# Optimization experiments

Hardware: AMD Instinct MI355X
Metric: run time of the kernel (lower is better)

The kernel has to match this reference:

```python
import jax, jax.numpy as jnp
import numpy as np

CH = 64          # channels
OC = 64          # out_channels
B, H, W = 8, 128, 128
NCA_C = CH + OC  # 128, NCA state channels
K = 3            # kernel_size
DILS = (1, 2, 4, 8)
HID = 64         # NCA update hidden
EPS = 1e-5


def setup_inputs() -> dict:
    key = jax.random.key(0)
    ks = jax.random.split(key, 16)
    def n(k, shape, s=0.02):
        return jax.random.normal(k, shape, jnp.float32) * s
    return {
        "x": jax.random.normal(ks[0], (B, H, W, CH), jnp.float32),
        "c": jax.random.normal(ks[1], (B, OC), jnp.float32),
        # Attention params
        "Wq": n(ks[2], (CH, OC)), "bq": jnp.zeros((OC,), jnp.float32),
        "Wk": n(ks[3], (OC, OC)), "bk": jnp.zeros((OC,), jnp.float32),
        "Wv": n(ks[4], (OC, OC)), "bv": jnp.zeros((OC,), jnp.float32),
        "Wo": n(ks[5], (OC, OC)), "bo": jnp.zeros((OC,), jnp.float32),
        "ln_g": jnp.ones((OC,), jnp.float32), "ln_b": jnp.zeros((OC,), jnp.float32),
        # NCA depthwise perception kernels, one per dilation: [4, NCA_C, 1, K, K]
        "pk": n(ks[6], (len(DILS), NCA_C, 1, K, K), 0.1),
        # NCA update MLP
        "W1": n(ks[7], ((1 + len(DILS)) * NCA_C, HID)), "b1": jnp.zeros((HID,), jnp.float32),
        "W2": n(ks[8], (HID, CH)), "b2": jnp.zeros((CH,), jnp.float32),
    }


def _layernorm(z, g, b):
    m = jnp.mean(z, axis=-1, keepdims=True)
    v = jnp.var(z, axis=-1, keepdims=True)
    return (z - m) / jnp.sqrt(v + EPS) * g + b


def _forward(x, c, Wq, bq, Wk, bk, Wv, bv, Wo, bo, ln_g, ln_b, pk, W1, b1, W2, b2):
    b_, h_, w_, _ = x.shape
    # ---- Attention(x, c): single-key softmax pooling over H*W ----
    q = x.reshape(b_, h_ * w_, CH) @ Wq + bq              # [B, HW, OC]
    k = c @ Wk + bk                                        # [B, OC]
    v = c @ Wv + bv                                        # [B, OC]
    scores = jnp.einsum('bno,bo->bn', q, k) * (OC ** -0.5)  # [B, HW]
    attn = jax.nn.softmax(scores, axis=1)                  # softmax over spatial dim
    attended = jnp.einsum('bn,bo->bo', attn, v)            # weighted pool (weights sum to 1)
    a = _layernorm(attended @ Wo + bo + c, ln_g, ln_b)     # out_proj + residual + LN
    c2 = c + a                                             # outer residual in NCAAttention

    # ---- concat broadcast context -> NCA state [B,H,W,NCA_C] ----
    c_exp = jnp.broadcast_to(c2[:, None, None, :], (b_, h_, w_, OC))
    xc = jnp.concatenate([x, c_exp], axis=-1)

    # ---- NCA perception: depthwise dilated convs (SAME padding) ----
    xp = jnp.transpose(xc, (0, 3, 1, 2))                   # NCHW
    feats = [xc]
    for i, d in enumerate(DILS):
        pad = d * (K // 2)
        p = jax.lax.conv_general_dilated(
            xp, pk[i], window_strides=(1, 1),
            padding=[(pad, pad), (pad, pad)], rhs_dilation=(d, d),
            dimension_numbers=('NCHW', 'OIHW', 'NCHW'),
            feature_group_count=NCA_C)
        feats.append(jnp.transpose(p, (0, 2, 3, 1)))
    upd_in = jnp.concatenate(feats, axis=-1)               # [B,H,W,5*NCA_C]

    # ---- NCA update MLP: Linear -> (Dropout=id) -> GELU -> Linear ----
    hidden = jax.nn.gelu(upd_in @ W1 + b1, approximate=False)
    y = hidden @ W2 + b2                                   # [B,H,W,CH]
    # NCA.out_channels (64) != NCA.channels (128) -> no residual add
    return y, c2


def reference(x, c, Wq, bq, Wk, bk, Wv, bv, Wo, bo, ln_g, ln_b, pk, W1, b1, W2, b2):
    return _forward(x, c, Wq, bq, Wk, bk, Wv, bv, Wo, bo, ln_g, ln_b, pk, W1, b1, W2, b2)
```

## Files before the change

### kernel.cpp

```cpp
#include <hip/hip_runtime.h>
#include <hip/hip_bf16.h>
#include <math.h>


typedef float  f32x4 __attribute__((ext_vector_type(4)));
typedef short  s16x8 __attribute__((ext_vector_type(8)));

static __device__ __forceinline__ unsigned short f2bf(float f) {
    __hip_bfloat16 h = __float2bfloat16(f);
    unsigned short u; __builtin_memcpy(&u, &h, 2); return u;
}

#define XROW   2304
#define XPLANE 331776
#define XBATCH 1327104

__global__ void prepA(const float* __restrict__ x, const float* __restrict__ c,
                      const float* __restrict__ Wv, const float* __restrict__ bv,
                      const float* __restrict__ Wo, const float* __restrict__ bo,
                      const float* __restrict__ lng, const float* __restrict__ lnb,
                      unsigned short* __restrict__ xp, float* __restrict__ c2f,
                      float* __restrict__ outc2)
{
    const int blk = blockIdx.x, tid = threadIdx.x;
    if (blk < 512) {
        int i = blk*256 + tid;
        int xc = i & 127, y = (i >> 7) & 127, b = i >> 14;
        const float* src = x + (size_t)i*64;
        unsigned short* dstb = xp + ((size_t)b*4*144 + (y+8))*XROW + (xc+8)*16;
        #pragma unroll
        for (int p = 0; p < 4; ++p) {
            float4 f0 = *(const float4*)(src + p*16 + 0);
            float4 f1 = *(const float4*)(src + p*16 + 4);
            float4 f2 = *(const float4*)(src + p*16 + 8);
            float4 f3 = *(const float4*)(src + p*16 + 12);
            uint4 o0, o1;
            o0.x = (unsigned)f2bf(f0.x) | ((unsigned)f2bf(f0.y) << 16);
            o0.y = (unsigned)f2bf(f0.z) | ((unsigned)f2bf(f0.w) << 16);
            o0.z = (unsigned)f2bf(f1.x) | ((unsigned)f2bf(f1.y) << 16);
            o0.w = (unsigned)f2bf(f1.z) | ((unsigned)f2bf(f1.w) << 16);
            o1.x = (unsigned)f2bf(f2.x) | ((unsigned)f2bf(f2.y) << 16);
            o1.y = (unsigned)f2bf(f2.z) | ((unsigned)f2bf(f2.w) << 16);
            o1.z = (unsigned)f2bf(f3.x) | ((unsigned)f2bf(f3.y) << 16);
            o1.w = (unsigned)f2bf(f3.z) | ((unsigned)f2bf(f3.w) << 16);
            unsigned short* d = dstb + (size_t)p*XPLANE;
            *(uint4*)d = o0; *(uint4*)(d + 8) = o1;
        }
    } else if (blk < 1056) {
        int idx = (blk - 512)*256 + tid;
        int bp = idx / 4352;
        int r  = idx - bp*4352;
        int yy, xx;
        if (r < 2304) { int ry = r / 144; xx = r - ry*144; yy = (ry < 8) ? ry : 128 + ry; }
        else { int r2 = r - 2304; yy = 8 + (r2 >> 4); int xi = r2 & 15; xx = (xi < 8) ? xi : 128 + xi; }
        uint4 z = make_uint4(0,0,0,0);
        unsigned short* d = xp + ((size_t)bp*144 + yy)*XROW + xx*16;
        *(uint4*)d = z; *(uint4*)(d + 8) = z;
    } else {
        const int b = blk - 1056;
        __shared__ float sc[64], sv[64];
        const int j = tid;
        if (j < 64) sc[j] = c[b*64 + j];
        __syncthreads();
        if (j < 64) {
            float v = bv[j];
            for (int i = 0; i < 64; ++i) v += sc[i]*Wv[i*64 + j];
            sv[j] = v;
        }
        __syncthreads();
        if (j < 64) {
            float t = bo[j] + sc[j];
            for (int i = 0; i < 64; ++i) t += sv[i]*Wo[i*64 + j];
            float s = t;
            for (int o = 32; o > 0; o >>= 1) s += __shfl_xor(s, o);
            float m = s * (1.f/64.f);
            float dq = (t - m)*(t - m);
            for (int o = 32; o > 0; o >>= 1) dq += __shfl_xor(dq, o);
            float a = (t - m) / sqrtf(dq*(1.f/64.f) + 1e-5f) * lng[j] + lnb[j];
            float c2 = sc[j] + a;
            c2f[b*64 + j] = c2;
            outc2[b*64 + j] = c2;
        }
    }
}

__global__ void prepB(const float* __restrict__ pk, const float* __restrict__ W1,
                      const float* __restrict__ W2, const float* __restrict__ b1,
                      const float* __restrict__ c2f,
                      unsigned short* __restrict__ Uf, unsigned short* __restrict__ W2s,
                      float* __restrict__ V, float* __restrict__ hcp)
{
    const int blk = blockIdx.x, tid = threadIdx.x;
    if (blk < 74) {
        int idx = blk*256 + tid;
        int lane = idx & 63, nt = (idx >> 6) & 3, kc2 = (idx >> 8) & 1, pos = idx >> 9;
        int n  = nt*16 + (lane & 15);
        int k0 = kc2*32 + (lane >> 4)*8;
        unsigned short e[8];
        if (pos == 0) {
            #pragma unroll
            for (int j = 0; j < 8; ++j) e[j] = f2bf(W1[(k0+j)*64 + n]);
        } else {
            int di = (pos-1)/9, t = (pos-1)%9;
            #pragma unroll
            for (int j = 0; j < 8; ++j) {
                int ch = k0 + j;
                e[j] = f2bf(pk[(di*128 + ch)*9 + t] * W1[((1+di)*128 + ch)*64 + n]);
            }
        }
        uint4 o;
        o.x = (unsigned)e[0] | ((unsigned)e[1] << 16);
        o.y = (unsigned)e[2] | ((unsigned)e[3] << 16);
        o.z = (unsigned)e[4] | ((unsigned)e[5] << 16);
        o.w = (unsigned)e[6] | ((unsigned)e[7] << 16);
        *(uint4*)(Uf + (size_t)idx*8) = o;
    } else if (blk < 76) {
        int idx = (blk-74)*256 + tid;
        int lane = idx & 63, nt = (idx >> 6) & 3, kc2 = (idx >> 8) & 1;
        int n  = nt*16 + (lane & 15);
        int k0 = kc2*32 + (lane >> 4)*8;
        unsigned short e[8];
        #pragma unroll
        for (int j = 0; j < 8; ++j) e[j] = f2bf(W2[(k0+j)*64 + n]);
        uint4 o;
        o.x = (unsigned)e[0] | ((unsigned)e[1] << 16);
        o.y = (unsigned)e[2] | ((unsigned)e[3] << 16);
        o.z = (unsigned)e[4] | ((unsigned)e[5] << 16);
        o.w = (unsigned)e[6] | ((unsigned)e[7] << 16);
        *(uint4*)(W2s + (size_t)idx*8) = o;
    } else if (blk < 148) {
        int idx = (blk-76)*256 + tid;
        int n = idx & 63, q = idx >> 6;
        int p = q % 36, b = q / 36;
        int di = p/9, t = p%9;
        float s = 0.f;
        for (int j = 0; j < 64; ++j)
            s += c2f[b*64 + j] * pk[(di*128 + 64 + j)*9 + t] * W1[((1+di)*128 + 64 + j)*64 + n];
        V[(size_t)q*64 + n] = s;
    } else {
        for (int it = tid; it < 512; it += 256) {
            int b = it >> 6, n = it & 63;
            float s = b1[n];
            for (int j = 0; j < 64; ++j) s += c2f[b*64 + j]*W1[(64 + j)*64 + n];
            hcp[it] = s;
        }
    }
}

#define HID_S 72

__global__ __launch_bounds__(256) void nca_main(
    const unsigned short* __restrict__ xp,
    const unsigned short* __restrict__ U,
    const unsigned short* __restrict__ W2s,
    const float* __restrict__ V,
    const float* __restrict__ hcp,
    const float* __restrict__ b2,
    float* __restrict__ out)
{
    __shared__ float V_l[36*64];
    __shared__ float Cx_l[16*64];
    __shared__ float Cy_l[2*64];
    __shared__ float hc2_l[64];
    __shared__ unsigned short hid[256*HID_S];

    const int tid = threadIdx.x;
    const int blk = blockIdx.x;
    const int b  = blk & 7;
    const int y0 = (blk >> 3) * 2;

    {
        const float4* Vg = (const float4*)(V + (size_t)b*2304);
        for (int i = tid; i < 576; i += 256) ((float4*)V_l)[i] = Vg[i];
    }
    __syncthreads();
    for (int it = tid; it < 1024; it += 256) {
        int xi = it >> 6, n = it & 63;
        int xx = xi < 8 ? xi : 112 + xi;
        float s = 0.f;
        #pragma unroll
        for (int di = 0; di < 4; ++di) {
            int d = 1 << di;
            int dxo = (xx < d) ? 0 : ((xx >= 128 - d) ? 2 : -1);
            if (dxo >= 0) {
                s += V_l[(di*9 + 0*3 + dxo)*64 + n];
                s += V_l[(di*9 + 1*3 + dxo)*64 + n];
                s += V_l[(di*9 + 2*3 + dxo)*64 + n];
            }
        }
        Cx_l[it] = s;
    }
    for (int it = tid; it < 128; it += 256) {
        int r = it >> 6, n = it & 63;
        int yy = y0 + r;
        float s = 0.f;
        #pragma unroll
        for (int di = 0; di < 4; ++di) {
            int d = 1 << di;
            int dyo = (yy < d) ? 0 : ((yy >= 128 - d) ? 2 : -1);
            if (dyo >= 0) {
                s += V_l[(di*9 + dyo*3 + 0)*64 + n];
                s += V_l[(di*9 + dyo*3 + 1)*64 + n];
                s += V_l[(di*9 + dyo*3 + 2)*64 + n];
            }
        }
        Cy_l[it] = s;
    }
    if (tid < 64) {
        float s = hcp[b*64 + tid];
        for (int p = 0; p < 36; ++p) s += V_l[p*64 + tid];
        hc2_l[tid] = s;
    }
    __syncthreads();

    const int lane = tid & 63;
    const int w    = tid >> 6;
    const int y    = y0 + (w >> 1);
    const int xw   = (w & 1) * 64;
    const int ln15 = lane & 15;
    const int oct  = lane >> 4;

    const unsigned short* base0 = xp + (size_t)b*XBATCH + (size_t)(oct >> 1)*XPLANE
                                + (size_t)(y + 8)*XROW + (size_t)(xw + ln15 + 8)*16
                                + (oct & 1)*8;

    f32x4 acc[4][4];
    #pragma unroll
    for (int mt = 0; mt < 4; ++mt)
        #pragma unroll
        for (int nt = 0; nt < 4; ++nt) {
            acc[mt][nt][0] = 0.f; acc[mt][nt][1] = 0.f;
            acc[mt][nt][2] = 0.f; acc[mt][nt][3] = 0.f;
        }

    static constexpr int OFF[37] = {
        0,
        (-1*144-1)*16, (-1*144)*16, (-1*144+1)*16,
        (-1)*16,       0*16,        (1)*16,
        ( 1*144-1)*16, ( 1*144)*16, ( 1*144+1)*16,
        (-2*144-2)*16, (-2*144)*16, (-2*144+2)*16,
        (-2)*16,       0*16,        (2)*16,
        ( 2*144-2)*16, ( 2*144)*16, ( 2*144+2)*16,
        (-4*144-4)*16, (-4*144)*16, (-4*144+4)*16,
        (-4)*16,       0*16,        (4)*16,
        ( 4*144-4)*16, ( 4*144)*16, ( 4*144+4)*16,
        (-8*144-8)*16, (-8*144)*16, (-8*144+8)*16,
        (-8)*16,       0*16,        (8)*16,
        ( 8*144-8)*16, ( 8*144)*16, ( 8*144+8)*16
    };

    s16x8 avc[2][4];
    #pragma unroll
    for (int kc2 = 0; kc2 < 2; ++kc2)
        #pragma unroll
        for (int mt = 0; mt < 4; ++mt)
            avc[kc2][mt] = *(const s16x8*)(base0 + OFF[0] + kc2*(2*XPLANE) + mt*256);

    #pragma unroll 1
    for (int pos = 0; pos < 37; ++pos) {
        s16x8 avn[2][4];
        if (pos < 36) {
            const unsigned short* rp = base0 + OFF[pos + 1];
            #pragma unroll
            for (int kc2 = 0; kc2 < 2; ++kc2)
                #pragma unroll
                for (int mt = 0; mt < 4; ++mt)
                    avn[kc2][mt] = *(const s16x8*)(rp + kc2*(2*XPLANE) + mt*256);
        }
        const unsigned short* Up = U + (size_t)pos*4096 + lane*8;
        #pragma unroll
        for (int kc2 = 0; kc2 < 2; ++kc2) {
            #pragma unroll
            for (int nt = 0; nt < 4; ++nt) {
                s16x8 bf = *(const s16x8*)(Up + kc2*2048 + nt*512);
                #pragma unroll
                for (int mt = 0; mt < 4; ++mt)
                    acc[mt][nt] = __builtin_amdgcn_mfma_f32_16x16x32_bf16(avc[kc2][mt], bf, acc[mt][nt], 0, 0, 0);
            }
        }
        #pragma unroll
        for (int kc2 = 0; kc2 < 2; ++kc2)
            #pragma unroll
            for (int mt = 0; mt < 4; ++mt)
                avc[kc2][mt] = avn[kc2][mt];
    }

    const bool yedge = (y < 8) || (y >= 120);
    #pragma unroll
    for (int mt = 0; mt < 4; ++mt) {
        #pragma unroll
        for (int nt = 0; nt < 4; ++nt) {
            const int n = nt*16 + ln15;
            const float hcv = hc2_l[n];
            const float cyv = yedge ? Cy_l[(w >> 1)*64 + n] : 0.f;
            #pragma unroll
            for (int r = 0; r < 4; ++r) {
                int m = oct*4 + r;
                int x = xw + mt*16 + m;
                float h = acc[mt][nt][r] + hcv - cyv;
                if (x < 8 || x >= 120) {
                    int xi = (x < 8) ? x : (x - 112);
                    h -= Cx_l[xi*64 + n];
                    if (yedge) {
                        #pragma unroll
                        for (int di = 0; di < 4; ++di) {
                            int d = 1 << di;
                            int dyo = (y < d) ? 0 : ((y >= 128 - d) ? 2 : -1);
                            int dxo = (x < d) ? 0 : ((x >= 128 - d) ? 2 : -1);
                            if (dyo >= 0 && dxo >= 0)
                                h += V_l[(di*9 + dyo*3 + dxo)*64 + n];
                        }
                    }
                }
                float u = 0.7978845608028654f * (h + 0.044715f*h*h*h);
                float g = h / (1.f + __expf(-2.f*u));
                hid[(w*64 + mt*16 + m)*HID_S + n] = f2bf(g);
            }
        }
    }

    f32x4 acc2[4][4];
    #pragma unroll
    for (int mt = 0; mt < 4; ++mt)
        #pragma unroll
        for (int nt = 0; nt < 4; ++nt) {
            acc2[mt][nt][0] = 0.f; acc2[mt][nt][1] = 0.f;
            acc2[mt][nt][2] = 0.f; acc2[mt][nt][3] = 0.f;
        }
    #pragma unroll
    for (int kc2 = 0; kc2 < 2; ++kc2) {
        s16x8 a2[4];
        #pragma unroll
        for (int mt = 0; mt < 4; ++mt)
            a2[mt] = *(const s16x8*)&hid[(w*64 + mt*16 + ln15)*HID_S + kc2*32 + oct*8];
        #pragma unroll
        for (int nt = 0; nt < 4; ++nt) {
            s16x8 bf = *(const s16x8*)(W2s + ((size_t)(kc2*4 + nt)*64 + lane)*8);
            #pragma unroll
            for (int mt = 0; mt < 4; ++mt)
                acc2[mt][nt] = __builtin_amdgcn_mfma_f32_16x16x32_bf16(a2[mt], bf, acc2[mt][nt], 0, 0, 0);
        }
    }

    float* ob = out + ((size_t)(b*128 + y))*128*64;
    #pragma unroll
    for (int nt = 0; nt < 4; ++nt) {
        const float b2v = b2[nt*16 + ln15];
        #pragma unroll
        for (int mt = 0; mt < 4; ++mt) {
            #pragma unroll
            for (int r = 0; r < 4; ++r) {
                int x = xw + mt*16 + oct*4 + r;
                ob[(size_t)x*64 + nt*16 + ln15] = acc2[mt][nt][r] + b2v;
            }
        }
    }
}

extern "C" void kernel_launch(void* const* d_in, const int* in_sizes, int n_in,
                              void* d_out, int out_size, void* d_ws, size_t ws_size,
                              hipStream_t stream) {
    const float* x   = (const float*)d_in[0];
    const float* c   = (const float*)d_in[1];
    const float* Wv  = (const float*)d_in[6];
    const float* bv  = (const float*)d_in[7];
    const float* Wo  = (const float*)d_in[8];
    const float* bo  = (const float*)d_in[9];
    const float* lng = (const float*)d_in[10];
    const float* lnb = (const float*)d_in[11];
    const float* pk  = (const float*)d_in[12];
    const float* W1  = (const float*)d_in[13];
    const float* b1  = (const float*)d_in[14];
    const float* W2  = (const float*)d_in[15];
    const float* b2  = (const float*)d_in[16];
    float* out = (float*)d_out;

    char* w = (char*)d_ws;
    unsigned short* xpb = (unsigned short*)(w);
    unsigned short* Uf  = (unsigned short*)(w + 21233664);
    unsigned short* W2s = (unsigned short*)(w + 21536768);
    float*          V   = (float*)         (w + 21544960);
    float*          hcp = (float*)         (w + 21618688);
    float*          c2f = (float*)         (w + 21620736);

    prepA<<<1064, 256, 0, stream>>>(x, c, Wv, bv, Wo, bo, lng, lnb, xpb, c2f, out + 8388608);
    prepB<<<149, 256, 0, stream>>>(pk, W1, W2, b1, c2f, Uf, W2s, V, hcp);
    nca_main<<<512, 256, 0, stream>>>(xpb, Uf, W2s, V, hcp, b2, out);
}
```

Before: 179.4 us.

## Stage U weight chunks through double-buffered LDS instead of global reads

```diff
diff --git a/kernel.cpp b/kernel.cpp
--- a/kernel.cpp
+++ b/kernel.cpp
@@ -158,11 +158,11 @@
     const float* __restrict__ b2,
     float* __restrict__ out)
 {
+    __shared__ unsigned short pool[32768];
     __shared__ float V_l[36*64];
     __shared__ float Cx_l[16*64];
     __shared__ float Cy_l[2*64];
     __shared__ float hc2_l[64];
-    __shared__ unsigned short hid[256*HID_S];
 
     const int tid = threadIdx.x;
     const int blk = blockIdx.x;
@@ -172,6 +172,10 @@
     {
         const float4* Vg = (const float4*)(V + (size_t)b*2304);
         for (int i = tid; i < 576; i += 256) ((float4*)V_l)[i] = Vg[i];
+        const uint4* Ug = (const uint4*)U;
+        uint4* dst = (uint4*)pool;
+        #pragma unroll
+        for (int i = 0; i < 8; ++i) dst[i*256 + tid] = Ug[i*256 + tid];
     }
     __syncthreads();
     for (int it = tid; it < 1024; it += 256) {
@@ -257,17 +261,55 @@
             avc[kc2][mt] = *(const s16x8*)(base0 + OFF[0] + kc2*(2*XPLANE) + mt*256);
 
     #pragma unroll 1
-    for (int pos = 0; pos < 37; ++pos) {
-        s16x8 avn[2][4];
-        if (pos < 36) {
-            const unsigned short* rp = base0 + OFF[pos + 1];
+    for (int ci = 0; ci < 9; ++ci) {
+        const int nsw = (ci == 8) ? 2 : 8;
+        uint4 st[8];
+        {
+            const uint4* src = (const uint4*)(U + (size_t)(ci + 1)*16384);
+            #pragma unroll
+            for (int i = 0; i < 8; ++i)
+                if (i < nsw) st[i] = src[i*256 + tid];
+        }
+        unsigned short* Ul = pool + (ci & 1)*16384;
+        #pragma unroll
+        for (int j = 0; j < 4; ++j) {
+            const int pos = ci*4 + j;
+            s16x8 avn[2][4];
+            {
+                const unsigned short* rp = base0 + OFF[pos + 1];
+                #pragma unroll
+                for (int kc2 = 0; kc2 < 2; ++kc2)
+                    #pragma unroll
+                    for (int mt = 0; mt < 4; ++mt)
+                        avn[kc2][mt] = *(const s16x8*)(rp + kc2*(2*XPLANE) + mt*256);
+            }
+            const unsigned short* Up = Ul + j*4096 + lane*8;
+            #pragma unroll
+            for (int kc2 = 0; kc2 < 2; ++kc2) {
+                #pragma unroll
+                for (int nt = 0; nt < 4; ++nt) {
+                    s16x8 bf = *(const s16x8*)(Up + kc2*2048 + nt*512);
+                    #pragma unroll
+                    for (int mt = 0; mt < 4; ++mt)
+                        acc[mt][nt] = __builtin_amdgcn_mfma_f32_16x16x32_bf16(avc[kc2][mt], bf, acc[mt][nt], 0, 0, 0);
+                }
+            }
             #pragma unroll
             for (int kc2 = 0; kc2 < 2; ++kc2)
                 #pragma unroll
                 for (int mt = 0; mt < 4; ++mt)
-                    avn[kc2][mt] = *(const s16x8*)(rp + kc2*(2*XPLANE) + mt*256);
-        }
-        const unsigned short* Up = U + (size_t)pos*4096 + lane*8;
+                    avc[kc2][mt] = avn[kc2][mt];
+        }
+        {
+            uint4* dst = (uint4*)(pool + ((ci + 1) & 1)*16384);
+            #pragma unroll
+            for (int i = 0; i < 8; ++i)
+                if (i < nsw) dst[i*256 + tid] = st[i];
+        }
+        __syncthreads();
+    }
+    {
+        const unsigned short* Up = pool + 16384 + lane*8;
         #pragma unroll
         for (int kc2 = 0; kc2 < 2; ++kc2) {
             #pragma unroll
@@ -278,13 +320,10 @@
                     acc[mt][nt] = __builtin_amdgcn_mfma_f32_16x16x32_bf16(avc[kc2][mt], bf, acc[mt][nt], 0, 0, 0);
             }
         }
-        #pragma unroll
-        for (int kc2 = 0; kc2 < 2; ++kc2)
-            #pragma unroll
-            for (int mt = 0; mt < 4; ++mt)
-                avc[kc2][mt] = avn[kc2][mt];
-    }
-
+    }
+    __syncthreads();
+
+    unsigned short* hid = pool;
     const bool yedge = (y < 8) || (y >= 120);
     #pragma unroll
     for (int mt = 0; mt < 4; ++mt) {
@@ -378,10 +417,10 @@
     char* w = (char*)d_ws;
     unsigned short* xpb = (unsigned short*)(w);
     unsigned short* Uf  = (unsigned short*)(w + 21233664);
-    unsigned short* W2s = (unsigned short*)(w + 21536768);
-    float*          V   = (float*)         (w + 21544960);
-    float*          hcp = (float*)         (w + 21618688);
-    float*          c2f = (float*)         (w + 21620736);
+    unsigned short* W2s = (unsigned short*)(w + 21561344);
+    float*          V   = (float*)         (w + 21569536);
+    float*          hcp = (float*)         (w + 21643264);
+    float*          c2f = (float*)         (w + 21645312);
 
     prepA<<<1064, 256, 0, stream>>>(x, c, Wv, bv, Wo, bo, lng, lnb, xpb, c2f, out + 8388608);
     prepB<<<149, 256, 0, stream>>>(pk, W1, W2, b1, c2f, Uf, W2s, V, hcp);
```

Result: slower. 201.5 us (+12.4%).

## Quantize padded input and fused conv weights to FP8, merge center taps

Applied to the files above, without the earlier changes.

```diff
diff --git a/kernel.cpp b/kernel.cpp
--- a/kernel.cpp
+++ b/kernel.cpp
@@ -5,21 +5,29 @@
 
 typedef float  f32x4 __attribute__((ext_vector_type(4)));
 typedef short  s16x8 __attribute__((ext_vector_type(8)));
+typedef long   i64;
 
 static __device__ __forceinline__ unsigned short f2bf(float f) {
     __hip_bfloat16 h = __float2bfloat16(f);
     unsigned short u; __builtin_memcpy(&u, &h, 2); return u;
 }
+static __device__ __forceinline__ unsigned pk4fp8(float f0, float f1, float f2, float f3) {
+    int v = 0;
+    v = __builtin_amdgcn_cvt_pk_fp8_f32(f0, f1, v, false);
+    v = __builtin_amdgcn_cvt_pk_fp8_f32(f2, f3, v, true);
+    return (unsigned)v;
+}
 
 #define XROW   2304
 #define XPLANE 331776
 #define XBATCH 1327104
+#define USCALE 256.0f
 
 __global__ void prepA(const float* __restrict__ x, const float* __restrict__ c,
                       const float* __restrict__ Wv, const float* __restrict__ bv,
                       const float* __restrict__ Wo, const float* __restrict__ bo,
                       const float* __restrict__ lng, const float* __restrict__ lnb,
-                      unsigned short* __restrict__ xp, float* __restrict__ c2f,
+                      unsigned char* __restrict__ xp, float* __restrict__ c2f,
                       float* __restrict__ outc2)
 {
     const int blk = blockIdx.x, tid = threadIdx.x;
@@ -27,24 +35,19 @@
         int i = blk*256 + tid;
         int xc = i & 127, y = (i >> 7) & 127, b = i >> 14;
         const float* src = x + (size_t)i*64;
-        unsigned short* dstb = xp + ((size_t)b*4*144 + (y+8))*XROW + (xc+8)*16;
+        unsigned char* dstb = xp + ((size_t)b*4*144 + (y+8))*XROW + (xc+8)*16;
         #pragma unroll
         for (int p = 0; p < 4; ++p) {
             float4 f0 = *(const float4*)(src + p*16 + 0);
             float4 f1 = *(const float4*)(src + p*16 + 4);
             float4 f2 = *(const float4*)(src + p*16 + 8);
             float4 f3 = *(const float4*)(src + p*16 + 12);
-            uint4 o0, o1;
-            o0.x = (unsigned)f2bf(f0.x) | ((unsigned)f2bf(f0.y) << 16);
-            o0.y = (unsigned)f2bf(f0.z) | ((unsigned)f2bf(f0.w) << 16);
-            o0.z = (unsigned)f2bf(f1.x) | ((unsigned)f2bf(f1.y) << 16);
-            o0.w = (unsigned)f2bf(f1.z) | ((unsigned)f2bf(f1.w) << 16);
-            o1.x = (unsigned)f2bf(f2.x) | ((unsigned)f2bf(f2.y) << 16);
-            o1.y = (unsigned)f2bf(f2.z) | ((unsigned)f2bf(f2.w) << 16);
-            o1.z = (unsigned)f2bf(f3.x) | ((unsigned)f2bf(f3.y) << 16);
-            o1.w = (unsigned)f2bf(f3.z) | ((unsigned)f2bf(f3.w) << 16);
-            unsigned short* d = dstb + (size_t)p*XPLANE;
-            *(uint4*)d = o0; *(uint4*)(d + 8) = o1;
+            uint4 o;
+            o.x = pk4fp8(f0.x, f0.y, f0.z, f0.w);
+            o.y = pk4fp8(f1.x, f1.y, f1.z, f1.w);
+            o.z = pk4fp8(f2.x, f2.y, f2.z, f2.w);
+            o.w = pk4fp8(f3.x, f3.y, f3.z, f3.w);
+            *(uint4*)(dstb + (size_t)p*XPLANE) = o;
         }
     } else if (blk < 1056) {
         int idx = (blk - 512)*256 + tid;
@@ -53,9 +56,7 @@
         int yy, xx;
         if (r < 2304) { int ry = r / 144; xx = r - ry*144; yy = (ry < 8) ? ry : 128 + ry; }
         else { int r2 = r - 2304; yy = 8 + (r2 >> 4); int xi = r2 & 15; xx = (xi < 8) ? xi : 128 + xi; }
-        uint4 z = make_uint4(0,0,0,0);
-        unsigned short* d = xp + ((size_t)bp*144 + yy)*XROW + xx*16;
-        *(uint4*)d = z; *(uint4*)(d + 8) = z;
+        *(uint4*)(xp + ((size_t)bp*144 + yy)*XROW + xx*16) = make_uint4(0,0,0,0);
     } else {
         const int b = blk - 1056;
         __shared__ float sc[64], sv[64];
@@ -87,35 +88,40 @@
 __global__ void prepB(const float* __restrict__ pk, const float* __restrict__ W1,
                       const float* __restrict__ W2, const float* __restrict__ b1,
                       const float* __restrict__ c2f,
-                      unsigned short* __restrict__ Uf, unsigned short* __restrict__ W2s,
+                      unsigned char* __restrict__ Uf, unsigned short* __restrict__ W2s,
                       float* __restrict__ V, float* __restrict__ hcp)
 {
     const int blk = blockIdx.x, tid = threadIdx.x;
-    if (blk < 74) {
+    if (blk < 66) {
         int idx = blk*256 + tid;
         int lane = idx & 63, nt = (idx >> 6) & 3, kc2 = (idx >> 8) & 1, pos = idx >> 9;
         int n  = nt*16 + (lane & 15);
         int k0 = kc2*32 + (lane >> 4)*8;
-        unsigned short e[8];
-        if (pos == 0) {
-            #pragma unroll
-            for (int j = 0; j < 8; ++j) e[j] = f2bf(W1[(k0+j)*64 + n]);
-        } else {
-            int di = (pos-1)/9, t = (pos-1)%9;
-            #pragma unroll
-            for (int j = 0; j < 8; ++j) {
-                int ch = k0 + j;
-                e[j] = f2bf(pk[(di*128 + ch)*9 + t] * W1[((1+di)*128 + ch)*64 + n]);
-            }
-        }
-        uint4 o;
-        o.x = (unsigned)e[0] | ((unsigned)e[1] << 16);
-        o.y = (unsigned)e[2] | ((unsigned)e[3] << 16);
-        o.z = (unsigned)e[4] | ((unsigned)e[5] << 16);
-        o.w = (unsigned)e[6] | ((unsigned)e[7] << 16);
-        *(uint4*)(Uf + (size_t)idx*8) = o;
-    } else if (blk < 76) {
-        int idx = (blk-74)*256 + tid;
+        static constexpr int DI[33] = {3,3,3, 2,2,2, 1,1,1, 0,0,0, -1, 0,0, 1,1, 2,2, 3,3,
+                                       0,0,0, 1,1,1, 2,2,2, 3,3,3};
+        static constexpr int TT[33] = {0,1,2, 0,1,2, 0,1,2, 0,1,2, 4, 3,5, 3,5, 3,5, 3,5,
+                                       6,7,8, 6,7,8, 6,7,8, 6,7,8};
+        int di = DI[pos], t = TT[pos];
+        float vv[8];
+        #pragma unroll
+        for (int j = 0; j < 8; ++j) {
+            int ch = k0 + j;
+            float v;
+            if (di < 0) {
+                v = W1[ch*64 + n];
+                for (int dd = 0; dd < 4; ++dd)
+                    v += pk[(dd*128 + ch)*9 + 4] * W1[((1+dd)*128 + ch)*64 + n];
+            } else {
+                v = pk[(di*128 + ch)*9 + t] * W1[((1+di)*128 + ch)*64 + n];
+            }
+            vv[j] = v * USCALE;
+        }
+        uint2 o;
+        o.x = pk4fp8(vv[0], vv[1], vv[2], vv[3]);
+        o.y = pk4fp8(vv[4], vv[5], vv[6], vv[7]);
+        *(uint2*)(Uf + (size_t)idx*8) = o;
+    } else if (blk < 68) {
+        int idx = (blk-66)*256 + tid;
         int lane = idx & 63, nt = (idx >> 6) & 3, kc2 = (idx >> 8) & 1;
         int n  = nt*16 + (lane & 15);
         int k0 = kc2*32 + (lane >> 4)*8;
@@ -128,8 +134,8 @@
         o.z = (unsigned)e[4] | ((unsigned)e[5] << 16);
         o.w = (unsigned)e[6] | ((unsigned)e[7] << 16);
         *(uint4*)(W2s + (size_t)idx*8) = o;
-    } else if (blk < 148) {
-        int idx = (blk-76)*256 + tid;
+    } else if (blk < 140) {
+        int idx = (blk-68)*256 + tid;
         int n = idx & 63, q = idx >> 6;
         int p = q % 36, b = q / 36;
         int di = p/9, t = p%9;
@@ -150,19 +156,19 @@
 #define HID_S 72
 
 __global__ __launch_bounds__(256) void nca_main(
-    const unsigned short* __restrict__ xp,
-    const unsigned short* __restrict__ U,
+    const unsigned char* __restrict__ xp,
+    const unsigned char* __restrict__ U,
     const unsigned short* __restrict__ W2s,
     const float* __restrict__ V,
     const float* __restrict__ hcp,
     const float* __restrict__ b2,
     float* __restrict__ out)
 {
+    __shared__ unsigned short hid[256*HID_S];
     __shared__ float V_l[36*64];
     __shared__ float Cx_l[16*64];
     __shared__ float Cy_l[2*64];
     __shared__ float hc2_l[64];
-    __shared__ unsigned short hid[256*HID_S];
 
     const int tid = threadIdx.x;
     const int blk = blockIdx.x;
@@ -220,9 +226,9 @@
     const int ln15 = lane & 15;
     const int oct  = lane >> 4;
 
-    const unsigned short* base0 = xp + (size_t)b*XBATCH + (size_t)(oct >> 1)*XPLANE
-                                + (size_t)(y + 8)*XROW + (size_t)(xw + ln15 + 8)*16
-                                + (oct & 1)*8;
+    const unsigned char* base0 = xp + (size_t)b*XBATCH + (size_t)(oct >> 1)*XPLANE
+                               + (size_t)(y + 8)*XROW + (size_t)(xw + ln15 + 8)*16
+                               + (oct & 1)*8;
 
     f32x4 acc[4][4];
     #pragma unroll
@@ -233,49 +239,46 @@
             acc[mt][nt][2] = 0.f; acc[mt][nt][3] = 0.f;
         }
 
-    static constexpr int OFF[37] = {
+    static constexpr int OFF[33] = {
+        (-8*144-8)*16, (-8*144)*16, (-8*144+8)*16,
+        (-4*144-4)*16, (-4*144)*16, (-4*144+4)*16,
+        (-2*144-2)*16, (-2*144)*16, (-2*144+2)*16,
+        (-1*144-1)*16, (-1*144)*16, (-1*144+1)*16,
         0,
-        (-1*144-1)*16, (-1*144)*16, (-1*144+1)*16,
-        (-1)*16,       0*16,        (1)*16,
+        -1*16, 1*16, -2*16, 2*16, -4*16, 4*16, -8*16, 8*16,
         ( 1*144-1)*16, ( 1*144)*16, ( 1*144+1)*16,
-        (-2*144-2)*16, (-2*144)*16, (-2*144+2)*16,
-        (-2)*16,       0*16,        (2)*16,
         ( 2*144-2)*16, ( 2*144)*16, ( 2*144+2)*16,
-        (-4*144-4)*16, (-4*144)*16, (-4*144+4)*16,
-        (-4)*16,       0*16,        (4)*16,
         ( 4*144-4)*16, ( 4*144)*16, ( 4*144+4)*16,
-        (-8*144-8)*16, (-8*144)*16, (-8*144+8)*16,
-        (-8)*16,       0*16,        (8)*16,
         ( 8*144-8)*16, ( 8*144)*16, ( 8*144+8)*16
     };
 
-    s16x8 avc[2][4];
+    i64 avc[2][4];
     #pragma unroll
     for (int kc2 = 0; kc2 < 2; ++kc2)
         #pragma unroll
         for (int mt = 0; mt < 4; ++mt)
-            avc[kc2][mt] = *(const s16x8*)(base0 + OFF[0] + kc2*(2*XPLANE) + mt*256);
+            avc[kc2][mt] = *(const i64*)(base0 + OFF[0] + kc2*(2*XPLANE) + mt*256);
 
     #pragma unroll 1
-    for (int pos = 0; pos < 37; ++pos) {
-        s16x8 avn[2][4];
-        if (pos < 36) {
-            const unsigned short* rp = base0 + OFF[pos + 1];
+    for (int pos = 0; pos < 33; ++pos) {
+        i64 avn[2][4];
+        if (pos < 32) {
+            const unsigned char* rp = base0 + OFF[pos + 1];
             #pragma unroll
             for (int kc2 = 0; kc2 < 2; ++kc2)
                 #pragma unroll
                 for (int mt = 0; mt < 4; ++mt)
-                    avn[kc2][mt] = *(const s16x8*)(rp + kc2*(2*XPLANE) + mt*256);
-        }
-        const unsigned short* Up = U + (size_t)pos*4096 + lane*8;
+                    avn[kc2][mt] = *(const i64*)(rp + kc2*(2*XPLANE) + mt*256);
+        }
+        const unsigned char* Up = U + (size_t)pos*4096 + lane*8;
         #pragma unroll
         for (int kc2 = 0; kc2 < 2; ++kc2) {
             #pragma unroll
             for (int nt = 0; nt < 4; ++nt) {
-                s16x8 bf = *(const s16x8*)(Up + kc2*2048 + nt*512);
+                i64 bf = *(const i64*)(Up + kc2*2048 + nt*512);
                 #pragma unroll
                 for (int mt = 0; mt < 4; ++mt)
-                    acc[mt][nt] = __builtin_amdgcn_mfma_f32_16x16x32_bf16(avc[kc2][mt], bf, acc[mt][nt], 0, 0, 0);
+                    acc[mt][nt] = __builtin_amdgcn_mfma_f32_16x16x32_fp8_fp8(avc[kc2][mt], bf, acc[mt][nt], 0, 0, 0);
             }
         }
         #pragma unroll
@@ -297,7 +300,7 @@
             for (int r = 0; r < 4; ++r) {
                 int m = oct*4 + r;
                 int x = xw + mt*16 + m;
-                float h = acc[mt][nt][r] + hcv - cyv;
+                float h = acc[mt][nt][r]*(1.0f/USCALE) + hcv - cyv;
                 if (x < 8 || x >= 120) {
                     int xi = (x < 8) ? x : (x - 112);
                     h -= Cx_l[xi*64 + n];
@@ -376,14 +379,14 @@
     float* out = (float*)d_out;
 
     char* w = (char*)d_ws;
-    unsigned short* xpb = (unsigned short*)(w);
-    unsigned short* Uf  = (unsigned short*)(w + 21233664);
-    unsigned short* W2s = (unsigned short*)(w + 21536768);
-    float*          V   = (float*)         (w + 21544960);
-    float*          hcp = (float*)         (w + 21618688);
-    float*          c2f = (float*)         (w + 21620736);
+    unsigned char*  xpb = (unsigned char*)(w);
+    unsigned char*  Uf  = (unsigned char*)(w + 10616832);
+    unsigned short* W2s = (unsigned short*)(w + 10752000);
+    float*          V   = (float*)         (w + 10760192);
+    float*          hcp = (float*)         (w + 10833920);
+    float*          c2f = (float*)         (w + 10835968);
 
     prepA<<<1064, 256, 0, stream>>>(x, c, Wv, bv, Wo, bo, lng, lnb, xpb, c2f, out + 8388608);
-    prepB<<<149, 256, 0, stream>>>(pk, W1, W2, b1, c2f, Uf, W2s, V, hcp);
+    prepB<<<141, 256, 0, stream>>>(pk, W1, W2, b1, c2f, Uf, W2s, V, hcp);
     nca_main<<<512, 256, 0, stream>>>(xpb, Uf, W2s, V, hcp, b2, out);
 }
```

New measurement: 167.8 us. 1.07x faster.
